# Optimization experiments

Measured on AMD Instinct MI355X. Metric: run time of the kernel, lower is better.

## Reference

```python
import jax, jax.numpy as jnp
import numpy as np

EPS = 1e-16


def setup_inputs() -> dict:
    key = jax.random.key(0)
    k1, k2 = jax.random.split(key)
    N, D = 512, 4096
    a = jax.random.normal(k1, (N, D), dtype=jnp.float32)
    p = jax.random.normal(k2, (N, D), dtype=jnp.float32)
    return {"a": a, "p": p}


def reference(a, p):
    N = a.shape[0]
    # Pairwise squared distances between anchors a and positives p:
    # ||a_i||^2 - 2 a_i . p_j + ||p_j||^2   (diag(a a^T) == row norms)
    dot = jnp.matmul(a, p.T)                       # [N, N]
    sq_a = jnp.sum(a * a, axis=-1)                 # [N]
    sq_p = jnp.sum(p * p, axis=-1)                 # [N]
    d2 = sq_a[:, None] - 2.0 * dot + sq_p[None, :]
    d2 = jnp.maximum(d2, 0.0)                      # distances[distances < 0] = 0
    zero_mask = (d2 == 0.0).astype(d2.dtype)
    dist = (1.0 - zero_mask) * jnp.sqrt(d2 + zero_mask * EPS)  # [N, N]

    # Triplet tensor: loss[a, p, n] = dist[a, p] - dist[a, n]
    triplet = dist[:, :, None] - dist[:, None, :]  # [N, N, N]

    # Validity mask: labels = arange(N) -> valid iff p == anchor and n != anchor
    labels = jnp.arange(N)
    label_eq = labels[:, None] == labels[None, :]  # [N, N]
    mask = label_eq[:, :, None] & (~label_eq[:, None, :])  # [N, N, N]

    triplet = mask.astype(triplet.dtype) * triplet
    triplet = jax.nn.relu(triplet)

    num_positive = jnp.sum(triplet > EPS).astype(triplet.dtype)
    loss = jnp.sum(triplet) / (num_positive + EPS)
    return loss
```

## Files before the change

kernel.cpp:

```cpp
#include <hip/hip_runtime.h>
#include <math.h>

#define PN 512
#define PD 4096

#define BK 256
#define NST (PD / BK)

#define WS_AH_BYTES 8192
#define WS_PH_BYTES (8192 + 4194304)
#define WS_NEED_MAIN ((size_t)(8192 + 2 * 4194304))

typedef __attribute__((ext_vector_type(8))) short short8;
typedef __attribute__((ext_vector_type(4))) float floatx4;

static __device__ __forceinline__ unsigned short f2bf(float x) {
    unsigned int u = __float_as_uint(x);
    u += 0x7fffu + ((u >> 16) & 1u);
    return (unsigned short)(u >> 16);
}

static __device__ __forceinline__ void load16_lds(const void* gp, void* lp) {
    __builtin_amdgcn_global_load_lds(
        (const __attribute__((address_space(1))) unsigned int*)gp,
        (__attribute__((address_space(3))) unsigned int*)lp,
        16, 0, 0);
}

struct ushort4s { unsigned short x, y, z, w; };

__global__ __launch_bounds__(256) void taw_prep_kernel(
        const float* __restrict__ a, const float* __restrict__ p,
        float* __restrict__ ws, int conv) {
    const int i = blockIdx.x;
    const int t = threadIdx.x;
    if (i == 0 && t == 0) {
        ws[1536] = 0.0f;
        ((unsigned int*)ws)[1537] = 0u;
        ((unsigned int*)ws)[1538] = 0u;
    }
    const float4* a4 = (const float4*)(a + (size_t)i * PD);
    const float4* p4 = (const float4*)(p + (size_t)i * PD);
    unsigned short* ah = (unsigned short*)((char*)ws + WS_AH_BYTES) + (size_t)i * PD;
    unsigned short* ph = (unsigned short*)((char*)ws + WS_PH_BYTES) + (size_t)i * PD;
    float sa = 0.f, sp = 0.f, dp = 0.f;
#pragma unroll
    for (int c = 0; c < 4; ++c) {
        const int e = c * 256 + t;
        float4 av = a4[e];
        float4 pv = p4[e];
        sa += av.x * av.x + av.y * av.y + av.z * av.z + av.w * av.w;
        sp += pv.x * pv.x + pv.y * pv.y + pv.z * pv.z + pv.w * pv.w;
        dp += av.x * pv.x + av.y * pv.y + av.z * pv.z + av.w * pv.w;
        if (conv) {
            ushort4s ab = {f2bf(av.x), f2bf(av.y), f2bf(av.z), f2bf(av.w)};
            ushort4s pb = {f2bf(pv.x), f2bf(pv.y), f2bf(pv.z), f2bf(pv.w)};
            *(ushort4s*)(ah + (size_t)e * 4) = ab;
            *(ushort4s*)(ph + (size_t)e * 4) = pb;
        }
    }
#pragma unroll
    for (int off = 32; off > 0; off >>= 1) {
        sa += __shfl_down(sa, off, 64);
        sp += __shfl_down(sp, off, 64);
        dp += __shfl_down(dp, off, 64);
    }
    __shared__ float red[3][4];
    const int wave = t >> 6;
    if ((t & 63) == 0) { red[0][wave] = sa; red[1][wave] = sp; red[2][wave] = dp; }
    __syncthreads();
    if (t == 0) {
        sa = red[0][0] + red[0][1] + red[0][2] + red[0][3];
        sp = red[1][0] + red[1][1] + red[1][2] + red[1][3];
        dp = red[2][0] + red[2][1] + red[2][2] + red[2][3];
        float d2 = sa - 2.f * dp + sp;
        d2 = fmaxf(d2, 0.f);
        ws[i] = sa;
        ws[512 + i] = sp;
        ws[1024 + i] = (d2 == 0.f) ? 0.f : sqrtf(d2);
    }
}

__global__ __launch_bounds__(256) void taw_fused_kernel(
        float* __restrict__ ws, float* __restrict__ out) {
    __shared__ short lds[2][32][64][8];
    const unsigned short* ah = (const unsigned short*)((const char*)ws + WS_AH_BYTES);
    const unsigned short* ph = (const unsigned short*)((const char*)ws + WS_PH_BYTES);
    const int t = threadIdx.x;
    const int lane = t & 63;
    const int w = t >> 6;
    const int wm = w >> 1, wn = w & 1;

    const int B = blockIdx.x;
    const int xcd = B & 7;
    const int l = B >> 3;
    const int bi = ((xcd >> 1) << 2) + (l >> 3);
    const int bj = ((xcd & 1) << 3) + (l & 7);
    const int i0 = bi * 32;
    const int j0 = bj * 32;

    const unsigned short* sbase[8];
#pragma unroll
    for (int q = 0; q < 8; ++q) {
        const int g16 = w * 8 + q;
        const int g = g16 & 15;
        const int row = ((g & 1) << 4) + (lane & 15);
        const int kk = ((g >> 1) << 5) + ((lane >> 4) << 3);
        sbase[q] = (g16 < 16 ? ah + (size_t)(i0 + row) * PD
                             : ph + (size_t)(j0 + row) * PD) + kk;
    }

    auto STAGE = [&](int buf, int kst) {
#pragma unroll
        for (int q = 0; q < 8; ++q) {
            load16_lds(sbase[q] + kst, &lds[buf][w * 8 + q][0][0]);
        }
    };

    floatx4 acc[4];
#pragma unroll
    for (int c = 0; c < 4; ++c) acc[c] = (floatx4){0.f, 0.f, 0.f, 0.f};

    STAGE(0, 0);
    __syncthreads();
    for (int st = 0; st < NST; ++st) {
        if (st + 1 < NST) STAGE((st + 1) & 1, (st + 1) * BK);
        const int b = st & 1;
#pragma unroll
        for (int kb = 0; kb < 8; ++kb) {
            short8 af = *(const short8*)&lds[b][kb * 2 + wm][lane][0];
            short8 bf = *(const short8*)&lds[b][16 + kb * 2 + wn][lane][0];
            acc[kb & 3] = __builtin_amdgcn_mfma_f32_16x16x32_bf16(af, bf, acc[kb & 3], 0, 0, 0);
        }
        __syncthreads();
    }

    const floatx4 dot = acc[0] + acc[1] + acc[2] + acc[3];

    const int jj = j0 + wn * 16 + (lane & 15);
    const int ib = i0 + wm * 16 + ((lane >> 4) << 2);
    const float sp = ws[512 + jj];
    float lsum = 0.f;
    unsigned int lcnt = 0;
#pragma unroll
    for (int r = 0; r < 4; ++r) {
        const int ii = ib + r;
        float d2 = ws[ii] - 2.f * dot[r] + sp;
        d2 = fmaxf(d2, 0.f);
        const float dist = (d2 == 0.f) ? 0.f : sqrtf(d2);
        const float v = (ii != jj) ? fmaxf(ws[1024 + ii] - dist, 0.f) : 0.f;
        lsum += v;
        lcnt += (v > 1e-16f) ? 1u : 0u;
    }
#pragma unroll
    for (int off = 32; off > 0; off >>= 1) {
        lsum += __shfl_down(lsum, off, 64);
        lcnt += __shfl_down(lcnt, off, 64);
    }
    __shared__ float rsum[4];
    __shared__ unsigned int rcnt[4];
    if ((t & 63) == 0) { rsum[w] = lsum; rcnt[w] = lcnt; }
    __syncthreads();
    if (t == 0) {
        atomicAdd(ws + 1536, rsum[0] + rsum[1] + rsum[2] + rsum[3]);
        atomicAdd(((unsigned int*)ws) + 1537, rcnt[0] + rcnt[1] + rcnt[2] + rcnt[3]);
        __threadfence();
        const unsigned int old = atomicAdd(((unsigned int*)ws) + 1538, 1u);
        if (old == 255u) {
            const float s = atomicAdd(ws + 1536, 0.f);
            const unsigned int c = atomicAdd(((unsigned int*)ws) + 1537, 0u);
            out[0] = (float)((double)s / ((double)c + 1e-16));
        }
    }
}

__global__ void taw_finalize_kernel(const float* __restrict__ ws,
                                    float* __restrict__ out) {
    const double s = (double)ws[1536];
    const double c = (double)(((const unsigned int*)ws)[1537]);
    out[0] = (float)(s / (c + 1e-16));
}

__global__ __launch_bounds__(256) void taw_gemm_loss_kernel(
        const float* __restrict__ A, const float* __restrict__ P,
        float* __restrict__ ws) {
    __shared__ float as[32][34];
    __shared__ float bs[32][34];
    const int tx = threadIdx.x;
    const int ty = threadIdx.y;
    const int t = ty * 16 + tx;
    const int i0 = blockIdx.y * 32;
    const int j0 = blockIdx.x * 32;
    const int sr = t >> 3;
    const int sk = (t & 7) * 4;
    const float* aptr = A + (size_t)(i0 + sr) * PD + sk;
    const float* pptr = P + (size_t)(j0 + sr) * PD + sk;
    float c00 = 0.f, c01 = 0.f, c10 = 0.f, c11 = 0.f;
    for (int k0 = 0; k0 < PD; k0 += 32) {
        float4 av = *(const float4*)(aptr + k0);
        float4 pv = *(const float4*)(pptr + k0);
        __syncthreads();
        as[sk + 0][sr] = av.x; as[sk + 1][sr] = av.y;
        as[sk + 2][sr] = av.z; as[sk + 3][sr] = av.w;
        bs[sk + 0][sr] = pv.x; bs[sk + 1][sr] = pv.y;
        bs[sk + 2][sr] = pv.z; bs[sk + 3][sr] = pv.w;
        __syncthreads();
#pragma unroll
        for (int kk = 0; kk < 32; ++kk) {
            const float2 a2 = *(const float2*)&as[kk][2 * ty];
            const float2 b2 = *(const float2*)&bs[kk][2 * tx];
            c00 = fmaf(a2.x, b2.x, c00);
            c01 = fmaf(a2.x, b2.y, c01);
            c10 = fmaf(a2.y, b2.x, c10);
            c11 = fmaf(a2.y, b2.y, c11);
        }
    }
    const float* sq_a = ws;
    const float* sq_p = ws + 512;
    const float* ddg  = ws + 1024;
    const int i = i0 + 2 * ty;
    const int j = j0 + 2 * tx;
    float cvals[2][2] = {{c00, c01}, {c10, c11}};
    float lsum = 0.f;
    unsigned int lcnt = 0;
#pragma unroll
    for (int dr = 0; dr < 2; ++dr)
#pragma unroll
        for (int dc = 0; dc < 2; ++dc) {
            const int ii = i + dr, jj = j + dc;
            float d2 = sq_a[ii] - 2.f * cvals[dr][dc] + sq_p[jj];
            d2 = fmaxf(d2, 0.f);
            const float dist = (d2 == 0.f) ? 0.f : sqrtf(d2);
            const float v = (ii != jj) ? fmaxf(ddg[ii] - dist, 0.f) : 0.f;
            lsum += v;
            lcnt += (v > 1e-16f) ? 1u : 0u;
        }
#pragma unroll
    for (int off = 32; off > 0; off >>= 1) {
        lsum += __shfl_down(lsum, off, 64);
        lcnt += __shfl_down(lcnt, off, 64);
    }
    __shared__ float rsum[4];
    __shared__ unsigned int rcnt[4];
    if ((t & 63) == 0) { rsum[t >> 6] = lsum; rcnt[t >> 6] = lcnt; }
    __syncthreads();
    if (t == 0) {
        atomicAdd(ws + 1536, rsum[0] + rsum[1] + rsum[2] + rsum[3]);
        atomicAdd(((unsigned int*)ws) + 1537, rcnt[0] + rcnt[1] + rcnt[2] + rcnt[3]);
    }
}

extern "C" void kernel_launch(void* const* d_in, const int* in_sizes, int n_in,
                              void* d_out, int out_size, void* d_ws, size_t ws_size,
                              hipStream_t stream) {
    (void)in_sizes; (void)n_in; (void)out_size;
    const float* a = (const float*)d_in[0];
    const float* p = (const float*)d_in[1];
    float* out = (float*)d_out;
    float* ws = (float*)d_ws;

    const int use_mfma = (ws_size >= WS_NEED_MAIN) ? 1 : 0;
    taw_prep_kernel<<<PN, 256, 0, stream>>>(a, p, ws, use_mfma);
    if (use_mfma) {
        taw_fused_kernel<<<256, 256, 0, stream>>>(ws, out);
    } else {
        taw_gemm_loss_kernel<<<dim3(16, 16), dim3(16, 16), 0, stream>>>(a, p, ws);
        taw_finalize_kernel<<<1, 1, 0, stream>>>(ws, out);
    }
}
```

Baseline: 101.8 us.

## Triple-buffer LDS staging and split K across waves in fused GEMM-loss kernel

Moves the fused kernel from double to triple-buffered LDS staging with explicit vmcnt waits, so loads run two stages ahead instead of one. The work split also changes: each wave now computes the full 32x32 tile over its own K slice (a 2x2 MFMA register block), and the partial sums are reduced through LDS afterwards. This is meant to hide global-to-LDS latency and raise MFMA issue density per fragment load. In exchange it needs more LDS (three buffers), adds an LDS reduction step, and relies on hand-written waitcnt/barrier sequencing that must match the number of loads issued per stage.

```diff
diff --git a/kernel.cpp b/kernel.cpp
--- a/kernel.cpp
+++ b/kernel.cpp
@@ -83,13 +83,12 @@
 
 __global__ __launch_bounds__(256) void taw_fused_kernel(
         float* __restrict__ ws, float* __restrict__ out) {
-    __shared__ short lds[2][32][64][8];
+    __shared__ short lds[3][32][64][8];
     const unsigned short* ah = (const unsigned short*)((const char*)ws + WS_AH_BYTES);
     const unsigned short* ph = (const unsigned short*)((const char*)ws + WS_PH_BYTES);
     const int t = threadIdx.x;
     const int lane = t & 63;
     const int w = t >> 6;
-    const int wm = w >> 1, wn = w & 1;
 
     const int B = blockIdx.x;
     const int xcd = B & 7;
@@ -117,35 +116,67 @@
         }
     };
 
-    floatx4 acc[4];
-#pragma unroll
-    for (int c = 0; c < 4; ++c) acc[c] = (floatx4){0.f, 0.f, 0.f, 0.f};
+    floatx4 acc[2][2];
+#pragma unroll
+    for (int rm = 0; rm < 2; ++rm)
+#pragma unroll
+        for (int rn = 0; rn < 2; ++rn) acc[rm][rn] = (floatx4){0.f, 0.f, 0.f, 0.f};
 
     STAGE(0, 0);
+    STAGE(1, BK);
+    for (int st = 0; st < NST; ++st) {
+        const int b = st - (st / 3) * 3;
+        if (st + 2 < NST) {
+            STAGE(st + 2 - ((st + 2) / 3) * 3, (st + 2) * BK);
+            asm volatile("s_waitcnt vmcnt(16)" ::: "memory");
+        } else if (st + 1 < NST) {
+            asm volatile("s_waitcnt vmcnt(8)" ::: "memory");
+        } else {
+            asm volatile("s_waitcnt vmcnt(0)" ::: "memory");
+        }
+        __builtin_amdgcn_s_barrier();
+        __builtin_amdgcn_sched_barrier(0);
+#pragma unroll
+        for (int c = 0; c < 2; ++c) {
+            const int kb = 2 * w + c;
+            short8 a0 = *(const short8*)&lds[b][2 * kb + 0][lane][0];
+            short8 a1 = *(const short8*)&lds[b][2 * kb + 1][lane][0];
+            short8 p0 = *(const short8*)&lds[b][16 + 2 * kb + 0][lane][0];
+            short8 p1 = *(const short8*)&lds[b][16 + 2 * kb + 1][lane][0];
+            acc[0][0] = __builtin_amdgcn_mfma_f32_16x16x32_bf16(a0, p0, acc[0][0], 0, 0, 0);
+            acc[0][1] = __builtin_amdgcn_mfma_f32_16x16x32_bf16(a0, p1, acc[0][1], 0, 0, 0);
+            acc[1][0] = __builtin_amdgcn_mfma_f32_16x16x32_bf16(a1, p0, acc[1][0], 0, 0, 0);
+            acc[1][1] = __builtin_amdgcn_mfma_f32_16x16x32_bf16(a1, p1, acc[1][1], 0, 0, 0);
+        }
+        __builtin_amdgcn_sched_barrier(0);
+        asm volatile("s_waitcnt lgkmcnt(0)" ::: "memory");
+        __builtin_amdgcn_s_barrier();
+    }
+
+    float* sc = (float*)&lds[0][0][0][0];
+#pragma unroll
+    for (int rm = 0; rm < 2; ++rm)
+#pragma unroll
+        for (int rn = 0; rn < 2; ++rn)
+#pragma unroll
+            for (int r = 0; r < 4; ++r)
+                sc[(((w * 2 + rm) * 2 + rn) * 4 + r) * 64 + lane] = acc[rm][rn][r];
     __syncthreads();
-    for (int st = 0; st < NST; ++st) {
-        if (st + 1 < NST) STAGE((st + 1) & 1, (st + 1) * BK);
-        const int b = st & 1;
-#pragma unroll
-        for (int kb = 0; kb < 8; ++kb) {
-            short8 af = *(const short8*)&lds[b][kb * 2 + wm][lane][0];
-            short8 bf = *(const short8*)&lds[b][16 + kb * 2 + wn][lane][0];
-            acc[kb & 3] = __builtin_amdgcn_mfma_f32_16x16x32_bf16(af, bf, acc[kb & 3], 0, 0, 0);
-        }
-        __syncthreads();
-    }
-
-    const floatx4 dot = acc[0] + acc[1] + acc[2] + acc[3];
-
-    const int jj = j0 + wn * 16 + (lane & 15);
-    const int ib = i0 + wm * 16 + ((lane >> 4) << 2);
-    const float sp = ws[512 + jj];
+
+    const int rm = w >> 1, rn = w & 1;
+    const int jj = j0 + rn * 16 + (lane & 15);
+    const int ib = i0 + rm * 16 + ((lane >> 4) << 2);
+    const float spv = ws[512 + jj];
     float lsum = 0.f;
     unsigned int lcnt = 0;
 #pragma unroll
     for (int r = 0; r < 4; ++r) {
+        const float dot = sc[(((0 * 2 + rm) * 2 + rn) * 4 + r) * 64 + lane]
+                        + sc[(((1 * 2 + rm) * 2 + rn) * 4 + r) * 64 + lane]
+                        + sc[(((2 * 2 + rm) * 2 + rn) * 4 + r) * 64 + lane]
+                        + sc[(((3 * 2 + rm) * 2 + rn) * 4 + r) * 64 + lane];
         const int ii = ib + r;
-        float d2 = ws[ii] - 2.f * dot[r] + sp;
+        float d2 = ws[ii] - 2.f * dot + spv;
         d2 = fmaxf(d2, 0.f);
         const float dist = (d2 == 0.f) ? 0.f : sqrtf(d2);
         const float v = (ii != jj) ? fmaxf(ws[1024 + ii] - dist, 0.f) : 0.f;
@@ -157,13 +188,13 @@
         lsum += __shfl_down(lsum, off, 64);
         lcnt += __shfl_down(lcnt, off, 64);
     }
-    __shared__ float rsum[4];
-    __shared__ unsigned int rcnt[4];
-    if ((t & 63) == 0) { rsum[w] = lsum; rcnt[w] = lcnt; }
+    float* rs = sc + 4096;
+    unsigned int* rc = (unsigned int*)(sc + 4100);
+    if ((t & 63) == 0) { rs[w] = lsum; rc[w] = lcnt; }
     __syncthreads();
     if (t == 0) {
-        atomicAdd(ws + 1536, rsum[0] + rsum[1] + rsum[2] + rsum[3]);
-        atomicAdd(((unsigned int*)ws) + 1537, rcnt[0] + rcnt[1] + rcnt[2] + rcnt[3]);
+        atomicAdd(ws + 1536, rs[0] + rs[1] + rs[2] + rs[3]);
+        atomicAdd(((unsigned int*)ws) + 1537, rc[0] + rc[1] + rc[2] + rc[3]);
         __threadfence();
         const unsigned int old = atomicAdd(((unsigned int*)ws) + 1538, 1u);
         if (old == 255u) {
```

After: 94.35 us. 1.08x faster.
